# Performance work log

Measured on AMD Instinct MI355X. Metric: run time of the kernel, lower is better.

Reference implementation:

```python
import jax, jax.numpy as jnp
import numpy as np

B, T, D, H = 2, 2048, 2048, 16
HD = D // H
EPS = 1e-8
NEG = -1e9


def setup_inputs() -> dict:
    key = jax.random.key(0)
    ks = jax.random.split(key, 6)
    x = jax.random.normal(ks[0], (B, T, D), dtype=jnp.float32)
    # additive causal mask, broadcast over [B, H, T, T]
    causal = jnp.tril(jnp.ones((T, T), dtype=bool))
    attn_mask = jnp.where(causal, 0.0, NEG).astype(jnp.float32)[None, None]
    s = 1.0 / np.sqrt(D)
    w_norm = jnp.ones((D,), dtype=jnp.float32)
    wq = jax.random.normal(ks[1], (D, D), dtype=jnp.float32) * s
    wk = jax.random.normal(ks[2], (D, D), dtype=jnp.float32) * s
    wv = jax.random.normal(ks[3], (D, D), dtype=jnp.float32) * s
    wo = jax.random.normal(ks[4], (D, D), dtype=jnp.float32) * s
    return {"x": x, "attn_mask": attn_mask, "w_norm": w_norm,
            "wq": wq, "wk": wk, "wv": wv, "wo": wo}


def _rmsnorm(x, w):
    # norm = ||x||_2 * D^-0.5 ; out = w * x / (norm + eps)  (eps outside, as in source)
    norm = jnp.sqrt(jnp.sum(x * x, axis=-1, keepdims=True)) * (x.shape[-1] ** -0.5)
    return w * x / (norm + EPS)


def reference(x, attn_mask, w_norm, wq, wk, wv, wo):
    b, t, d = x.shape
    xn = _rmsnorm(x, w_norm)
    # Linear (no bias): y = x @ W^T ; split into heads -> [B, H, T, HD]
    def proj(w):
        return jnp.einsum('btd,ed->bte', xn, w).reshape(b, t, H, HD).transpose(0, 2, 1, 3)
    q, k, v = proj(wq), proj(wk), proj(wv)
    scale = HD ** -0.5
    w_scores = jnp.einsum('bhqd,bhkd->bhqk', q, k) * scale + attn_mask
    p = jax.nn.softmax(w_scores, axis=-1)
    out = jnp.einsum('bhqk,bhkd->bhqd', p, v)
    out = out.transpose(0, 2, 1, 3).reshape(b, t, d)
    return jnp.einsum('btd,ed->bte', out, wo)
```

## Files before the change

### kernel.cpp

```cpp
#include <hip/hip_runtime.h>
#include <stdint.h>

#define TT 2048
#define DD 2048
#define NHH 16
#define HDD 128
#define BTT 4096

typedef __attribute__((ext_vector_type(8))) short bf16x8;
typedef __attribute__((ext_vector_type(4))) float f32x4;

#define MF(a, b, c) __builtin_amdgcn_mfma_f32_16x16x32_bf16(a, b, c, 0, 0, 0)

__device__ __forceinline__ unsigned short f2bf(float f) {
    union { float f; uint32_t u; } v; v.f = f;
    uint32_t u = v.u;
    u += 0x7fffu + ((u >> 16) & 1u);
    return (unsigned short)(u >> 16);
}

__device__ __forceinline__ void gld16(const unsigned short* g, unsigned short* l) {
    __builtin_amdgcn_global_load_lds(
        (const __attribute__((address_space(1))) unsigned int*)g,
        (__attribute__((address_space(3))) unsigned int*)l, 16, 0, 0);
}

__global__ __launch_bounds__(256) void convert_w(const float* __restrict__ wq,
                                                 const float* __restrict__ wk,
                                                 const float* __restrict__ wv,
                                                 const float* __restrict__ wo,
                                                 unsigned short* __restrict__ out) {
    size_t gid = (size_t)blockIdx.x * 256 + threadIdx.x;
    size_t base = gid * 8;
    int which = (int)(base >> 22);
    const float* src = which == 0 ? wq : which == 1 ? wk : which == 2 ? wv : wo;
    size_t off = base & 4194303u;
    float4 a = ((const float4*)(src + off))[0];
    float4 b = ((const float4*)(src + off))[1];
    union { unsigned short us[8]; uint4 v; } pk;
    pk.us[0] = f2bf(a.x); pk.us[1] = f2bf(a.y); pk.us[2] = f2bf(a.z); pk.us[3] = f2bf(a.w);
    pk.us[4] = f2bf(b.x); pk.us[5] = f2bf(b.y); pk.us[6] = f2bf(b.z); pk.us[7] = f2bf(b.w);
    *(uint4*)(out + base) = pk.v;
}

__global__ __launch_bounds__(256) void rmsnorm_k(const float* __restrict__ x,
                                                 const float* __restrict__ w,
                                                 unsigned short* __restrict__ xn) {
    const int row = blockIdx.x;
    const int tid = threadIdx.x;
    const float* xr = x + (size_t)row * DD;
    float4 a = ((const float4*)xr)[tid * 2];
    float4 b = ((const float4*)xr)[tid * 2 + 1];
    float ss = a.x*a.x + a.y*a.y + a.z*a.z + a.w*a.w
             + b.x*b.x + b.y*b.y + b.z*b.z + b.w*b.w;
    #pragma unroll
    for (int m = 1; m < 64; m <<= 1) ss += __shfl_xor(ss, m, 64);
    __shared__ float wss[4];
    if ((tid & 63) == 0) wss[tid >> 6] = ss;
    __syncthreads();
    float total = wss[0] + wss[1] + wss[2] + wss[3];
    float norm = sqrtf(total) * 0.022097086912079612f;
    float inv = 1.0f / (norm + 1e-8f);
    float4 wa = ((const float4*)w)[tid * 2];
    float4 wb = ((const float4*)w)[tid * 2 + 1];
    union { unsigned short us[8]; uint4 v; } pk;
    pk.us[0] = f2bf(wa.x * a.x * inv); pk.us[1] = f2bf(wa.y * a.y * inv);
    pk.us[2] = f2bf(wa.z * a.z * inv); pk.us[3] = f2bf(wa.w * a.w * inv);
    pk.us[4] = f2bf(wb.x * b.x * inv); pk.us[5] = f2bf(wb.y * b.y * inv);
    pk.us[6] = f2bf(wb.z * b.z * inv); pk.us[7] = f2bf(wb.w * b.w * inv);
    ((uint4*)(xn + (size_t)row * DD))[tid] = pk.v;
}

__device__ __forceinline__ void gemm128x256_core(const unsigned short* __restrict__ Ag,
                                                 const unsigned short* __restrict__ Bg,
                                                 unsigned short* lds, f32x4 acc[4][4]) {
    const int tid = threadIdx.x;
    const int wave = tid >> 6, lane = tid & 63;
    const int wm = wave >> 2, wn = wave & 3;
    const int l15 = lane & 15, lq = lane >> 4, r7 = l15 & 7;
    const int gr = lane >> 3;
    const size_t goff = (size_t)gr * DD + (size_t)(((lane & 7) ^ gr) * 8);
    const int xk0 = (lq ^ r7) * 8;
    const int xk1 = ((4 + lq) ^ r7) * 8;
    const int aro = (wm * 64 + l15) * 64;
    const int bro = 8192 + (wn * 64 + l15) * 64;
    const int swA = wave * 16;
    const int swB = wave * 32;

    #pragma unroll
    for (int c = 0; c < 2; c++)
        gld16(Ag + (size_t)(swA + c * 8) * DD + goff, lds + (swA + c * 8) * 64);
    #pragma unroll
    for (int c = 0; c < 4; c++)
        gld16(Bg + (size_t)(swB + c * 8) * DD + goff, lds + 8192 + (swB + c * 8) * 64);
    asm volatile("s_waitcnt vmcnt(0)" ::: "memory");
    __builtin_amdgcn_sched_barrier(0);
    __builtin_amdgcn_s_barrier();

    for (int kt = 0; kt < DD / 64; kt++) {
        const int cur = (kt & 1) ? 24576 : 0;
        const int nxt = 24576 - cur;
        const bool hn = (kt + 1 < DD / 64);
        const int kn = (kt + 1) * 64;
        const unsigned short* ac = lds + cur + aro;
        const unsigned short* bc = lds + cur + bro;
        bf16x8 afA[2][2], afB[2][2], bA[2][2], bB[2][2];

        #pragma unroll
        for (int m = 0; m < 2; m++) {
            afA[m][0] = *(const bf16x8*)(ac + m * 1024 + xk0);
            afA[m][1] = *(const bf16x8*)(ac + m * 1024 + xk1);
            afB[m][0] = *(const bf16x8*)(ac + (2 + m) * 1024 + xk0);
            afB[m][1] = *(const bf16x8*)(ac + (2 + m) * 1024 + xk1);
        }
        #pragma unroll
        for (int n = 0; n < 2; n++) {
            bA[n][0] = *(const bf16x8*)(bc + n * 1024 + xk0);
            bA[n][1] = *(const bf16x8*)(bc + n * 1024 + xk1);
        }
        if (hn) {
            #pragma unroll
            for (int c = 0; c < 2; c++)
                gld16(Ag + (size_t)(swA + c * 8) * DD + kn + goff,
                      lds + nxt + (swA + c * 8) * 64);
            #pragma unroll
            for (int c = 0; c < 4; c++)
                gld16(Bg + (size_t)(swB + c * 8) * DD + kn + goff,
                      lds + nxt + 8192 + (swB + c * 8) * 64);
        }
        __builtin_amdgcn_s_barrier();
        asm volatile("s_waitcnt lgkmcnt(0)" ::: "memory");
        __builtin_amdgcn_sched_barrier(0);
        __builtin_amdgcn_s_setprio(1);
        #pragma unroll
        for (int m = 0; m < 2; m++)
            #pragma unroll
            for (int n = 0; n < 2; n++) {
                acc[m][n]     = MF(afA[m][0], bA[n][0], acc[m][n]);
                acc[m][n]     = MF(afA[m][1], bA[n][1], acc[m][n]);
                acc[2 + m][n] = MF(afB[m][0], bA[n][0], acc[2 + m][n]);
                acc[2 + m][n] = MF(afB[m][1], bA[n][1], acc[2 + m][n]);
            }
        __builtin_amdgcn_s_setprio(0);
        __builtin_amdgcn_s_barrier();

        #pragma unroll
        for (int n = 0; n < 2; n++) {
            bB[n][0] = *(const bf16x8*)(bc + (2 + n) * 1024 + xk0);
            bB[n][1] = *(const bf16x8*)(bc + (2 + n) * 1024 + xk1);
        }
        __builtin_amdgcn_s_barrier();
        asm volatile("s_waitcnt lgkmcnt(0)" ::: "memory");
        __builtin_amdgcn_sched_barrier(0);
        __builtin_amdgcn_s_setprio(1);
        #pragma unroll
        for (int m = 0; m < 2; m++)
            #pragma unroll
            for (int n = 0; n < 2; n++) {
                acc[m][2 + n]     = MF(afA[m][0], bB[n][0], acc[m][2 + n]);
                acc[m][2 + n]     = MF(afA[m][1], bB[n][1], acc[m][2 + n]);
                acc[2 + m][2 + n] = MF(afB[m][0], bB[n][0], acc[2 + m][2 + n]);
                acc[2 + m][2 + n] = MF(afB[m][1], bB[n][1], acc[2 + m][2 + n]);
            }
        __builtin_amdgcn_s_setprio(0);
        asm volatile("s_waitcnt vmcnt(0)" ::: "memory");
        __builtin_amdgcn_sched_barrier(0);
        __builtin_amdgcn_s_barrier();
    }
}

__global__ __launch_bounds__(512, 2) void gemm_qkv(const unsigned short* __restrict__ A,
                                                   const unsigned short* __restrict__ W3,
                                                   unsigned short* __restrict__ O3) {
    __shared__ __align__(16) unsigned short lds[49152];
    const int orig = blockIdx.y * 32 + blockIdx.x;
    const int id = (orig & 7) * 96 + (orig >> 3);
    const int which = id >> 8;
    const int rem = id & 255;
    const int bn = rem >> 5, bm = rem & 31;
    const unsigned short* Bw = W3 + (size_t)which * DD * DD;
    unsigned short* C = O3 + (size_t)which * BTT * DD;
    const int m0 = bm * 128, n0 = bn * 256;
    const f32x4 zf = {0.f, 0.f, 0.f, 0.f};
    f32x4 acc[4][4];
    #pragma unroll
    for (int m = 0; m < 4; m++)
        #pragma unroll
        for (int n = 0; n < 4; n++) acc[m][n] = zf;
    gemm128x256_core(A + (size_t)m0 * DD, Bw + (size_t)n0 * DD, lds, acc);
    const int wave = threadIdx.x >> 6, lane = threadIdx.x & 63;
    const int wm = wave >> 2, wn = wave & 3;
    const int l15 = lane & 15, lq = lane >> 4;
    #pragma unroll
    for (int m = 0; m < 4; m++) {
        const int row = m0 + wm * 64 + m * 16 + lq * 4;
        #pragma unroll
        for (int n = 0; n < 4; n++) {
            const int col = n0 + wn * 64 + n * 16 + l15;
            #pragma unroll
            for (int r = 0; r < 4; r++)
                C[(size_t)(row + r) * DD + col] = f2bf(acc[m][n][r]);
        }
    }
}

__global__ __launch_bounds__(512, 2) void gemm_out(const unsigned short* __restrict__ A,
                                                   const unsigned short* __restrict__ Bw,
                                                   float* __restrict__ C) {
    __shared__ __align__(16) unsigned short lds[49152];
    const int orig = blockIdx.y * 32 + blockIdx.x;
    const int id = (orig & 7) * 32 + (orig >> 3);
    const int bn = id >> 5, bm = id & 31;
    const int m0 = bm * 128, n0 = bn * 256;
    const f32x4 zf = {0.f, 0.f, 0.f, 0.f};
    f32x4 acc[4][4];
    #pragma unroll
    for (int m = 0; m < 4; m++)
        #pragma unroll
        for (int n = 0; n < 4; n++) acc[m][n] = zf;
    gemm128x256_core(A + (size_t)m0 * DD, Bw + (size_t)n0 * DD, lds, acc);
    const int wave = threadIdx.x >> 6, lane = threadIdx.x & 63;
    const int wm = wave >> 2, wn = wave & 3;
    const int l15 = lane & 15, lq = lane >> 4;
    #pragma unroll
    for (int m = 0; m < 4; m++) {
        const int row = m0 + wm * 64 + m * 16 + lq * 4;
        #pragma unroll
        for (int n = 0; n < 4; n++) {
            const int col = n0 + wn * 64 + n * 16 + l15;
            #pragma unroll
            for (int r = 0; r < 4; r++)
                C[(size_t)(row + r) * DD + col] = acc[m][n][r];
        }
    }
}

__global__ __launch_bounds__(256) void attn_fused(const unsigned short* __restrict__ q,
                                                  const unsigned short* __restrict__ k,
                                                  const unsigned short* __restrict__ v,
                                                  unsigned short* __restrict__ o) {
    constexpr int LPP = 72;
    __shared__ __align__(16) unsigned short Ks[2][64 * 128];
    __shared__ __align__(16) unsigned short Vts[128 * 64];
    __shared__ __align__(16) unsigned short Ps[4 * 16 * LPP];
    const int h = blockIdx.y, b = blockIdx.z;
    const int tid = threadIdx.x, wave = tid >> 6, lane = tid & 63;
    const int l15 = lane & 15, lq = lane >> 4;
    const size_t rowbase = (size_t)b * TT;
    const int hcol = h * HDD;
    const float scale = 0.08838834764831845f;
    unsigned short* Pw = Ps + wave * 16 * LPP;
    const f32x4 zf = {0.f, 0.f, 0.f, 0.f};

    uint4 vr0, vr1, vr2, vr3;
    const int pr = tid >> 3;
    const int hc = (tid & 7) * 16;
    const int vsw0 = (2 * pr) ^ (((hc >> 3) & 7) << 3);
    const int vsw1 = (2 * pr) ^ ((((hc + 8) >> 3) & 7) << 3);

    const int klrow = lane >> 4;
    const int klch  = lane & 15;

    for (int half = 0; half < 2; half++) {
        const int qj = (half == 0) ? blockIdx.x : 31 - blockIdx.x;
        const int qt0 = qj * 64;
        bf16x8 aq[4];
        {
            const unsigned short* qrp = q + (rowbase + qt0 + wave * 16 + l15) * DD + hcol;
            #pragma unroll
            for (int kk = 0; kk < 4; kk++)
                aq[kk] = *(const bf16x8*)(qrp + kk * 32 + lq * 8);
        }
        f32x4 acc_o[8];
        #pragma unroll
        for (int jh = 0; jh < 8; jh++) acc_o[jh] = zf;
        float m_i[4], l_i[4];
        #pragma unroll
        for (int r = 0; r < 4; r++) { m_i[r] = -1e30f; l_i[r] = 0.f; }
        const int qp0 = qt0 + wave * 16 + lq * 4;
        const int nkt = qj + 1;

        __syncthreads();
        {
            const unsigned short* kg = k + rowbase * DD + hcol;
            const unsigned short* vg = v + rowbase * DD + hcol;
            #pragma unroll
            for (int i = 0; i < 4; i++) {
                const int r0 = wave * 16 + i * 4;
                const int row = r0 + klrow;
                const int gch = klch ^ (row & 7);
                gld16(kg + (size_t)row * DD + gch * 8, &Ks[0][r0 * 128]);
            }
            vr0 = *(const uint4*)(vg + (size_t)(2 * pr) * DD + hc);
            vr1 = *(const uint4*)(vg + (size_t)(2 * pr) * DD + hc + 8);
            vr2 = *(const uint4*)(vg + (size_t)(2 * pr + 1) * DD + hc);
            vr3 = *(const uint4*)(vg + (size_t)(2 * pr + 1) * DD + hc + 8);
        }

        for (int kt = 0; kt < nkt; kt++) {
            const int cur = kt & 1;
            __syncthreads();
            if (kt + 1 < nkt) {
                const unsigned short* kg = k + (rowbase + (kt + 1) * 64) * DD + hcol;
                #pragma unroll
                for (int i = 0; i < 4; i++) {
                    const int r0 = wave * 16 + i * 4;
                    const int row = r0 + klrow;
                    const int gch = klch ^ (row & 7);
                    gld16(kg + (size_t)row * DD + gch * 8, &Ks[cur ^ 1][r0 * 128]);
                }
            }
            {
                const unsigned short* s0 = (const unsigned short*)&vr0;
                const unsigned short* s1 = (const unsigned short*)&vr1;
                const unsigned short* s2 = (const unsigned short*)&vr2;
                const unsigned short* s3 = (const unsigned short*)&vr3;
                #pragma unroll
                for (int jj = 0; jj < 8; jj++) {
                    *(uint32_t*)(&Vts[(hc + jj) * 64 + vsw0]) =
                        (uint32_t)s0[jj] | ((uint32_t)s2[jj] << 16);
                    *(uint32_t*)(&Vts[(hc + 8 + jj) * 64 + vsw1]) =
                        (uint32_t)s1[jj] | ((uint32_t)s3[jj] << 16);
                }
            }
            if (kt + 1 < nkt) {
                const unsigned short* vg = v + (rowbase + (kt + 1) * 64) * DD + hcol;
                vr0 = *(const uint4*)(vg + (size_t)(2 * pr) * DD + hc);
                vr1 = *(const uint4*)(vg + (size_t)(2 * pr) * DD + hc + 8);
                vr2 = *(const uint4*)(vg + (size_t)(2 * pr + 1) * DD + hc);
                vr3 = *(const uint4*)(vg + (size_t)(2 * pr + 1) * DD + hc + 8);
            }
            const unsigned short* ksc = &Ks[cur][0];
            f32x4 accs[4];
            #pragma unroll
            for (int j = 0; j < 4; j++) accs[j] = zf;
            __builtin_amdgcn_s_setprio(1);
            #pragma unroll
            for (int j = 0; j < 4; j++)
                #pragma unroll
                for (int kk = 0; kk < 4; kk++) {
                    bf16x8 bk = *(const bf16x8*)(&ksc[(j * 16 + l15) * 128 +
                                                      (((kk * 4 + lq) ^ (l15 & 7)) * 8)]);
                    accs[j] = MF(aq[kk], bk, accs[j]);
                }
            __builtin_amdgcn_s_setprio(0);
            const int kbase = kt * 64;
            float rowmax[4] = {-1e30f, -1e30f, -1e30f, -1e30f};
            #pragma unroll
            for (int j = 0; j < 4; j++) {
                const int kp = kbase + j * 16 + l15;
                #pragma unroll
                for (int r = 0; r < 4; r++) {
                    float s = accs[j][r] * scale;
                    s = (kp > qp0 + r) ? -1e30f : s;
                    accs[j][r] = s;
                    rowmax[r] = fmaxf(rowmax[r], s);
                }
            }
            #pragma unroll
            for (int r = 0; r < 4; r++) {
                float mx = rowmax[r];
                mx = fmaxf(mx, __shfl_xor(mx, 1, 64));
                mx = fmaxf(mx, __shfl_xor(mx, 2, 64));
                mx = fmaxf(mx, __shfl_xor(mx, 4, 64));
                mx = fmaxf(mx, __shfl_xor(mx, 8, 64));
                float m_new = fmaxf(m_i[r], mx);
                float al = __expf(m_i[r] - m_new);
                m_i[r] = m_new;
                l_i[r] *= al;
                #pragma unroll
                for (int jh = 0; jh < 8; jh++) acc_o[jh][r] *= al;
            }
            float rowsum[4] = {0.f, 0.f, 0.f, 0.f};
            #pragma unroll
            for (int j = 0; j < 4; j++)
                #pragma unroll
                for (int r = 0; r < 4; r++) {
                    float p = __expf(accs[j][r] - m_i[r]);
                    rowsum[r] += p;
                    Pw[(lq * 4 + r) * LPP + j * 16 + l15] = f2bf(p);
                }
            #pragma unroll
            for (int r = 0; r < 4; r++) {
                float s = rowsum[r];
                s += __shfl_xor(s, 1, 64);
                s += __shfl_xor(s, 2, 64);
                s += __shfl_xor(s, 4, 64);
                s += __shfl_xor(s, 8, 64);
                l_i[r] += s;
            }
            __syncthreads();
            bf16x8 ap[2];
            #pragma unroll
            for (int kk = 0; kk < 2; kk++)
                ap[kk] = *(const bf16x8*)(&Pw[l15 * LPP + kk * 32 + lq * 8]);
            __builtin_amdgcn_s_setprio(1);
            #pragma unroll
            for (int jh = 0; jh < 8; jh++) {
                const int hd = jh * 16 + l15;
                const int vswz = ((hd >> 3) & 7) << 3;
                #pragma unroll
                for (int kk = 0; kk < 2; kk++) {
                    bf16x8 bv = *(const bf16x8*)(&Vts[hd * 64 + ((kk * 32 + lq * 8) ^ vswz)]);
                    acc_o[jh] = MF(ap[kk], bv, acc_o[jh]);
                }
            }
            __builtin_amdgcn_s_setprio(0);
        }
        #pragma unroll
        for (int jh = 0; jh < 8; jh++) {
            const int col = hcol + jh * 16 + l15;
            #pragma unroll
            for (int r = 0; r < 4; r++)
                o[(rowbase + qp0 + r) * DD + col] = f2bf(acc_o[jh][r] * (1.0f / l_i[r]));
        }
    }
}

extern "C" void kernel_launch(void* const* d_in, const int* in_sizes, int n_in,
                              void* d_out, int out_size, void* d_ws, size_t ws_size,
                              hipStream_t stream) {
    const float* x      = (const float*)d_in[0];
    const float* w_norm = (const float*)d_in[2];
    const float* wq     = (const float*)d_in[3];
    const float* wk     = (const float*)d_in[4];
    const float* wv     = (const float*)d_in[5];
    const float* wo     = (const float*)d_in[6];

    unsigned short* wbf = (unsigned short*)d_ws;
    unsigned short* xn  = wbf + (size_t)4 * DD * DD;
    unsigned short* qb  = xn + (size_t)BTT * DD;
    unsigned short* kb  = qb + (size_t)BTT * DD;
    unsigned short* vb  = kb + (size_t)BTT * DD;
    unsigned short* ab  = vb + (size_t)BTT * DD;

    convert_w<<<8192, 256, 0, stream>>>(wq, wk, wv, wo, wbf);
    rmsnorm_k<<<BTT, 256, 0, stream>>>(x, w_norm, xn);
    dim3 gqkv(32, 24);
    gemm_qkv<<<gqkv, 512, 0, stream>>>(xn, wbf, qb);
    dim3 gattn(16, NHH, 2);
    attn_fused<<<gattn, 256, 0, stream>>>(qb, kb, vb, ab);
    dim3 gout(32, 8);
    gemm_out<<<gout, 512, 0, stream>>>(ab, wbf + (size_t)3 * DD * DD, (float*)d_out);
}
```

Baseline: 426.8 us.

## Use triple-buffered LDS pipeline in GEMM core with single barrier per k-step

Replaces the double-buffered GEMM mainloop with a three-stage LDS ring, prefetching two k-tiles ahead and waiting with partial vmcnt. Each iteration now loads all A/B fragments at once and issues all 32 MFMAs in one block, cutting from three barriers per step to one. LDS per block grows from 96KB to 144KB, which may drop occupancy from the two blocks per CU requested by launch bounds, and the larger fragment set raises register pressure.

Result: faster. 412.4 us (-3.4%).

```diff
diff --git a/kernel.cpp b/kernel.cpp
--- a/kernel.cpp
+++ b/kernel.cpp
@@ -71,6 +71,18 @@
     ((uint4*)(xn + (size_t)row * DD))[tid] = pk.v;
 }
 
+__device__ __forceinline__ void stage_tile(const unsigned short* __restrict__ Ag,
+                                           const unsigned short* __restrict__ Bg,
+                                           int k0, unsigned short* buf,
+                                           int swA, int swB, size_t goff) {
+    #pragma unroll
+    for (int c = 0; c < 2; c++)
+        gld16(Ag + (size_t)(swA + c * 8) * DD + k0 + goff, buf + (swA + c * 8) * 64);
+    #pragma unroll
+    for (int c = 0; c < 4; c++)
+        gld16(Bg + (size_t)(swB + c * 8) * DD + k0 + goff, buf + 8192 + (swB + c * 8) * 64);
+}
+
 __device__ __forceinline__ void gemm128x256_core(const unsigned short* __restrict__ Ag,
                                                  const unsigned short* __restrict__ Bg,
                                                  unsigned short* lds, f32x4 acc[4][4]) {
@@ -86,93 +98,57 @@
     const int bro = 8192 + (wn * 64 + l15) * 64;
     const int swA = wave * 16;
     const int swB = wave * 32;
-
-    #pragma unroll
-    for (int c = 0; c < 2; c++)
-        gld16(Ag + (size_t)(swA + c * 8) * DD + goff, lds + (swA + c * 8) * 64);
-    #pragma unroll
-    for (int c = 0; c < 4; c++)
-        gld16(Bg + (size_t)(swB + c * 8) * DD + goff, lds + 8192 + (swB + c * 8) * 64);
-    asm volatile("s_waitcnt vmcnt(0)" ::: "memory");
+    unsigned short* p0 = lds;
+    unsigned short* p1 = lds + 24576;
+    unsigned short* p2 = lds + 49152;
+
+    stage_tile(Ag, Bg, 0, p0, swA, swB, goff);
+    stage_tile(Ag, Bg, 64, p1, swA, swB, goff);
+    asm volatile("s_waitcnt vmcnt(6)" ::: "memory");
     __builtin_amdgcn_sched_barrier(0);
     __builtin_amdgcn_s_barrier();
 
-    for (int kt = 0; kt < DD / 64; kt++) {
-        const int cur = (kt & 1) ? 24576 : 0;
-        const int nxt = 24576 - cur;
-        const bool hn = (kt + 1 < DD / 64);
-        const int kn = (kt + 1) * 64;
-        const unsigned short* ac = lds + cur + aro;
-        const unsigned short* bc = lds + cur + bro;
-        bf16x8 afA[2][2], afB[2][2], bA[2][2], bB[2][2];
-
-        #pragma unroll
-        for (int m = 0; m < 2; m++) {
-            afA[m][0] = *(const bf16x8*)(ac + m * 1024 + xk0);
-            afA[m][1] = *(const bf16x8*)(ac + m * 1024 + xk1);
-            afB[m][0] = *(const bf16x8*)(ac + (2 + m) * 1024 + xk0);
-            afB[m][1] = *(const bf16x8*)(ac + (2 + m) * 1024 + xk1);
-        }
-        #pragma unroll
-        for (int n = 0; n < 2; n++) {
-            bA[n][0] = *(const bf16x8*)(bc + n * 1024 + xk0);
-            bA[n][1] = *(const bf16x8*)(bc + n * 1024 + xk1);
-        }
-        if (hn) {
-            #pragma unroll
-            for (int c = 0; c < 2; c++)
-                gld16(Ag + (size_t)(swA + c * 8) * DD + kn + goff,
-                      lds + nxt + (swA + c * 8) * 64);
-            #pragma unroll
-            for (int c = 0; c < 4; c++)
-                gld16(Bg + (size_t)(swB + c * 8) * DD + kn + goff,
-                      lds + nxt + 8192 + (swB + c * 8) * 64);
-        }
-        __builtin_amdgcn_s_barrier();
+    for (int kt = 0; kt < 32; kt++) {
+        if (kt + 2 < 32)
+            stage_tile(Ag, Bg, (kt + 2) * 64, p2, swA, swB, goff);
+        const unsigned short* ac = p0 + aro;
+        const unsigned short* bc = p0 + bro;
+        bf16x8 a[4][2], b[4][2];
+        #pragma unroll
+        for (int m = 0; m < 4; m++) {
+            a[m][0] = *(const bf16x8*)(ac + m * 1024 + xk0);
+            a[m][1] = *(const bf16x8*)(ac + m * 1024 + xk1);
+        }
+        #pragma unroll
+        for (int n = 0; n < 4; n++) {
+            b[n][0] = *(const bf16x8*)(bc + n * 1024 + xk0);
+            b[n][1] = *(const bf16x8*)(bc + n * 1024 + xk1);
+        }
         asm volatile("s_waitcnt lgkmcnt(0)" ::: "memory");
         __builtin_amdgcn_sched_barrier(0);
         __builtin_amdgcn_s_setprio(1);
         #pragma unroll
-        for (int m = 0; m < 2; m++)
-            #pragma unroll
-            for (int n = 0; n < 2; n++) {
-                acc[m][n]     = MF(afA[m][0], bA[n][0], acc[m][n]);
-                acc[m][n]     = MF(afA[m][1], bA[n][1], acc[m][n]);
-                acc[2 + m][n] = MF(afB[m][0], bA[n][0], acc[2 + m][n]);
-                acc[2 + m][n] = MF(afB[m][1], bA[n][1], acc[2 + m][n]);
+        for (int m = 0; m < 4; m++)
+            #pragma unroll
+            for (int n = 0; n < 4; n++) {
+                acc[m][n] = MF(a[m][0], b[n][0], acc[m][n]);
+                acc[m][n] = MF(a[m][1], b[n][1], acc[m][n]);
             }
         __builtin_amdgcn_s_setprio(0);
+        if (kt + 1 < 32) {
+            if (kt + 2 < 32) { asm volatile("s_waitcnt vmcnt(6)" ::: "memory"); }
+            else             { asm volatile("s_waitcnt vmcnt(0)" ::: "memory"); }
+            __builtin_amdgcn_sched_barrier(0);
+        }
         __builtin_amdgcn_s_barrier();
-
-        #pragma unroll
-        for (int n = 0; n < 2; n++) {
-            bB[n][0] = *(const bf16x8*)(bc + (2 + n) * 1024 + xk0);
-            bB[n][1] = *(const bf16x8*)(bc + (2 + n) * 1024 + xk1);
-        }
-        __builtin_amdgcn_s_barrier();
-        asm volatile("s_waitcnt lgkmcnt(0)" ::: "memory");
-        __builtin_amdgcn_sched_barrier(0);
-        __builtin_amdgcn_s_setprio(1);
-        #pragma unroll
-        for (int m = 0; m < 2; m++)
-            #pragma unroll
-            for (int n = 0; n < 2; n++) {
-                acc[m][2 + n]     = MF(afA[m][0], bB[n][0], acc[m][2 + n]);
-                acc[m][2 + n]     = MF(afA[m][1], bB[n][1], acc[m][2 + n]);
-                acc[2 + m][2 + n] = MF(afB[m][0], bB[n][0], acc[2 + m][2 + n]);
-                acc[2 + m][2 + n] = MF(afB[m][1], bB[n][1], acc[2 + m][2 + n]);
-            }
-        __builtin_amdgcn_s_setprio(0);
-        asm volatile("s_waitcnt vmcnt(0)" ::: "memory");
-        __builtin_amdgcn_sched_barrier(0);
-        __builtin_amdgcn_s_barrier();
+        unsigned short* t = p0; p0 = p1; p1 = p2; p2 = t;
     }
 }
 
 __global__ __launch_bounds__(512, 2) void gemm_qkv(const unsigned short* __restrict__ A,
                                                    const unsigned short* __restrict__ W3,
                                                    unsigned short* __restrict__ O3) {
-    __shared__ __align__(16) unsigned short lds[49152];
+    __shared__ __align__(16) unsigned short lds[73728];
     const int orig = blockIdx.y * 32 + blockIdx.x;
     const int id = (orig & 7) * 96 + (orig >> 3);
     const int which = id >> 8;
@@ -207,7 +183,7 @@
 __global__ __launch_bounds__(512, 2) void gemm_out(const unsigned short* __restrict__ A,
                                                    const unsigned short* __restrict__ Bw,
                                                    float* __restrict__ C) {
-    __shared__ __align__(16) unsigned short lds[49152];
+    __shared__ __align__(16) unsigned short lds[73728];
     const int orig = blockIdx.y * 32 + blockIdx.x;
     const int id = (orig & 7) * 32 + (orig >> 3);
     const int bn = id >> 5, bm = id & 31;
```
